# Optimization experiments

Measured on AMD Instinct MI355X. Metric: run time of the kernel, lower is better.

## Reference

```python
import jax, jax.numpy as jnp
import numpy as np
from jax import lax


def setup_inputs() -> dict:
    key = jax.random.key(0)
    ks = jax.random.split(key, 8)
    b, l, d_model = 2, 1024, 768
    expand, d_state, d_conv = 2, 16, 4
    d_inner = d_model * expand            # 1536
    dt_rank = -(-d_model // 16)           # ceil(768/16) = 48
    x = jax.random.normal(ks[0], (b, l, d_model), jnp.float32)
    W_in = jax.random.normal(ks[1], (d_model, 2 * d_inner), jnp.float32) * 0.02
    conv_w = jax.random.normal(ks[2], (d_inner, 1, d_conv), jnp.float32) * 0.1
    conv_b = jnp.zeros((d_inner,), jnp.float32)
    W_x = jax.random.normal(ks[3], (d_inner, dt_rank + 2 * d_state), jnp.float32) * 0.02
    W_dt = jax.random.normal(ks[4], (dt_rank, d_inner), jnp.float32) * 0.02
    b_dt = jax.random.normal(ks[5], (d_inner,), jnp.float32) * 0.02
    # A_log = log(1..d_state) broadcast over d_inner, as in the module init
    A_log = jnp.broadcast_to(jnp.log(jnp.arange(1, d_state + 1, dtype=jnp.float32)), (d_inner, d_state)).copy()
    D = jnp.ones((d_inner,), jnp.float32)
    W_out = jax.random.normal(ks[6], (d_inner, d_model), jnp.float32) * 0.02
    return {"x": x, "W_in": W_in, "conv_w": conv_w, "conv_b": conv_b, "W_x": W_x,
            "W_dt": W_dt, "b_dt": b_dt, "A_log": A_log, "D": D, "W_out": W_out}


def _silu(v):
    return v * jax.nn.sigmoid(v)


def reference(x, W_in, conv_w, conv_b, W_x, W_dt, b_dt, A_log, D, W_out):
    b, l, d_model = x.shape
    d_inner, _, d_conv = conv_w.shape
    dt_rank = W_dt.shape[0]
    n = A_log.shape[1]

    # in_proj and split into x / res paths
    x_and_res = x @ W_in                              # (b, l, 2*d_inner)
    xi, res = jnp.split(x_and_res, 2, axis=-1)

    # depthwise causal conv1d (torch pads d_conv-1 both sides then slices [:l])
    xc = jnp.transpose(xi, (0, 2, 1))                 # (b, d_inner, l)
    xc = lax.conv_general_dilated(
        xc, conv_w, window_strides=(1,), padding=[(d_conv - 1, 0)],
        dimension_numbers=("NCH", "OIH", "NCH"), feature_group_count=d_inner)
    xc = xc + conv_b[None, :, None]
    u = _silu(jnp.transpose(xc, (0, 2, 1)))           # (b, l, d_inner)

    # SSM parameters (input-dependent)
    A = -jnp.exp(A_log.astype(jnp.float32))           # (d_inner, n)
    x_dbl = u @ W_x                                   # (b, l, dt_rank + 2n)
    delta = x_dbl[..., :dt_rank]
    B = x_dbl[..., dt_rank:dt_rank + n]               # (b, l, n)
    C = x_dbl[..., dt_rank + n:]                      # (b, l, n)
    delta = jax.nn.softplus(delta @ W_dt + b_dt)      # (b, l, d_inner)

    # discretize
    deltaA = jnp.exp(delta[..., None] * A)            # (b, l, d_inner, n)
    deltaB_u = delta[..., None] * B[:, :, None, :] * u[..., None]  # (b, l, d_inner, n)

    # parallel associative scan over l: h_t = deltaA_t * h_{t-1} + deltaB_u_t
    def combine(c1, c2):
        a1, b1 = c1
        a2, b2 = c2
        return (a1 * a2, a2 * b1 + b2)

    _, hs = lax.associative_scan(combine, (deltaA, deltaB_u), axis=1)  # (b, l, d_inner, n)

    y = jnp.einsum("bldn,bln->bld", hs, C) + u * D    # (b, l, d_inner)
    y = y * _silu(res)
    out = y @ W_out                                   # (b, l, d_model)
    return out
```

## Files before the change

### kernel.cpp

```cpp
#include <hip/hip_runtime.h>
#include <math.h>

#define DI 1536
#define DM 768
#define NSTATE 16
#define DTRANK 48
#define LSEQ 1024
#define NBATCH 2
#define MROWS (NBATCH*LSEQ)
#define NXR 3072
#define NCHUNK 64
#define CLEN 16
#define SCB 128
#define DMP 16

typedef __attribute__((ext_vector_type(4))) float f32x4;
typedef __attribute__((ext_vector_type(8))) short s16x8;
typedef __attribute__((ext_vector_type(4))) unsigned int u32x4;

__device__ __forceinline__ unsigned short f2bf(float f) {
  unsigned int x = __builtin_bit_cast(unsigned int, f);
  return (unsigned short)((x + 0x7fffu + ((x >> 16) & 1u)) >> 16);
}

__device__ __forceinline__ void gload_lds16(const void* g, void* l) {
  __builtin_amdgcn_global_load_lds(
      (const __attribute__((address_space(1))) void*)g,
      (__attribute__((address_space(3))) void*)l, 16, 0, 0);
}

__global__ __launch_bounds__(256) void convert_bf16_kernel(
    const float* __restrict__ in, unsigned short* __restrict__ out, long n)
{
  long i = ((long)blockIdx.x * 256 + threadIdx.x) * 8;
  if (i >= n) return;
  f32x4 v0 = *(const f32x4*)&in[i];
  f32x4 v1 = *(const f32x4*)&in[i + 4];
  unsigned short o[8];
  #pragma unroll
  for (int j = 0; j < 4; ++j) { o[j] = f2bf(v0[j]); o[4 + j] = f2bf(v1[j]); }
  *(u32x4*)&out[i] = *(u32x4*)o;
}

__global__ __launch_bounds__(256) void transpose_bf16_kernel(
    const float* __restrict__ in, unsigned short* __restrict__ out, int R, int C)
{
  __shared__ float t[32][33];
  int ctile = blockIdx.x * 32, rtile = blockIdx.y * 32;
  int tx = threadIdx.x & 31, ty = threadIdx.x >> 5;
  #pragma unroll
  for (int i = 0; i < 4; ++i) {
    int r = ty + i * 8;
    t[r][tx] = in[(long)(rtile + r) * C + ctile + tx];
  }
  __syncthreads();
  #pragma unroll
  for (int i = 0; i < 4; ++i) {
    int cc = ty + i * 8;
    out[(long)(ctile + cc) * R + rtile + tx] = f2bf(t[tx][cc]);
  }
}

__global__ __launch_bounds__(256) void transpose_bf16_guard(
    const float* __restrict__ in, unsigned short* __restrict__ out, int R, int C)
{
  __shared__ float t[32][33];
  int ctile = blockIdx.x * 32, rtile = blockIdx.y * 32;
  int tx = threadIdx.x & 31, ty = threadIdx.x >> 5;
  #pragma unroll
  for (int i = 0; i < 4; ++i) {
    int r = ty + i * 8;
    if (rtile + r < R && ctile + tx < C)
      t[r][tx] = in[(long)(rtile + r) * C + ctile + tx];
  }
  __syncthreads();
  #pragma unroll
  for (int i = 0; i < 4; ++i) {
    int cc = ty + i * 8;
    if (ctile + cc < C && rtile + tx < R)
      out[(long)(ctile + cc) * R + rtile + tx] = f2bf(t[tx][cc]);
  }
}

template<int FM, int FN>
__global__ __launch_bounds__(256) void gemm_bf16(
    const unsigned short* __restrict__ A,
    const unsigned short* __restrict__ BT,
    float* __restrict__ C, int M, int N, int K)
{
  constexpr int BM = 32 * FM, BN = 32 * FN;
  constexpr int TM = BM / 16, TN = BN / 16;
  __shared__ unsigned short Ap[BM * 32];
  __shared__ unsigned short Bp[BN * 32];
  const int tid = threadIdx.x;
  const int lane = tid & 63, wave = tid >> 6;
  const int wr = wave >> 1, wc = wave & 1;
  const int lg = lane >> 4, lr = lane & 15;
  const int m0 = blockIdx.y * BM, n0 = blockIdx.x * BN;
  f32x4 acc[FM][FN] = {};
  for (int k0 = 0; k0 < K; k0 += 32) {
    #pragma unroll
    for (int p = 0; p < TM / 4; ++p) {
      int tile = wave + p * 4;
      gload_lds16(&A[(long)(m0 + tile * 16 + lr) * K + k0 + lg * 8],
                  &Ap[tile * 512]);
    }
    #pragma unroll
    for (int p = 0; p < TN / 4; ++p) {
      int tile = wave + p * 4;
      gload_lds16(&BT[(long)(n0 + tile * 16 + lr) * K + k0 + lg * 8],
                  &Bp[tile * 512]);
    }
    __syncthreads();
    s16x8 af[FM], bfr[FN];
    #pragma unroll
    for (int m = 0; m < FM; ++m)
      af[m] = *(s16x8*)&Ap[(((wr * FM + m) * 4 + lg) * 16 + lr) * 8];
    #pragma unroll
    for (int n = 0; n < FN; ++n)
      bfr[n] = *(s16x8*)&Bp[(((wc * FN + n) * 4 + lg) * 16 + lr) * 8];
    #pragma unroll
    for (int m = 0; m < FM; ++m)
      #pragma unroll
      for (int n = 0; n < FN; ++n)
        acc[m][n] = __builtin_amdgcn_mfma_f32_16x16x32_bf16(af[m], bfr[n], acc[m][n], 0, 0, 0);
    __syncthreads();
  }
  #pragma unroll
  for (int m = 0; m < FM; ++m)
    #pragma unroll
    for (int n = 0; n < FN; ++n)
      #pragma unroll
      for (int r = 0; r < 4; ++r) {
        int row = m0 + wr * 16 * FM + m * 16 + lg * 4 + r;
        int col = n0 + wc * 16 * FN + n * 16 + lr;
        C[(long)row * N + col] = acc[m][n][r];
      }
}

__global__ __launch_bounds__(256) void conv_silu_kernel(
    const float* __restrict__ xr,
    const float* __restrict__ conv_w,
    const float* __restrict__ conv_b,
    float* __restrict__ u,
    unsigned short* __restrict__ u_bf)
{
  int idx = blockIdx.x * 256 + threadIdx.x;
  if (idx >= MROWS * DI) return;
  int c = idx % DI;
  int bm = idx / DI;
  int t = bm % LSEQ;
  int b = bm / LSEQ;
  float w0 = conv_w[c * 4 + 0], w1 = conv_w[c * 4 + 1];
  float w2 = conv_w[c * 4 + 2], w3 = conv_w[c * 4 + 3];
  const float* xc = xr + (long)b * LSEQ * NXR + c;
  float acc = conv_b[c];
  if (t >= 3) acc = fmaf(xc[(long)(t - 3) * NXR], w0, acc);
  if (t >= 2) acc = fmaf(xc[(long)(t - 2) * NXR], w1, acc);
  if (t >= 1) acc = fmaf(xc[(long)(t - 1) * NXR], w2, acc);
  acc = fmaf(xc[(long)t * NXR], w3, acc);
  float s = acc / (1.f + __expf(-acc));
  u[idx] = s;
  u_bf[idx] = f2bf(s);
}

__global__ __launch_bounds__(256) void xdbl_mfma(
    const unsigned short* __restrict__ u_bf,
    const unsigned short* __restrict__ WxT,
    float* __restrict__ xdbl)
{
  const int tid = threadIdx.x;
  const int lane = tid & 63, wave = tid >> 6;
  const int lg = lane >> 4, lr = lane & 15;
  const int m0 = blockIdx.x * 16;
  f32x4 acc[5] = {};
  const int kbase = wave * (DI / 4);
  #pragma unroll
  for (int kk = 0; kk < DI / 4; kk += 32) {
    int k0 = kbase + kk;
    s16x8 af = *(const s16x8*)&u_bf[(long)(m0 + lr) * DI + k0 + lg * 8];
    #pragma unroll
    for (int n = 0; n < 5; ++n) {
      s16x8 bfr = *(const s16x8*)&WxT[(long)(n * 16 + lr) * DI + k0 + lg * 8];
      acc[n] = __builtin_amdgcn_mfma_f32_16x16x32_bf16(af, bfr, acc[n], 0, 0, 0);
    }
  }
  __shared__ float red[4][16][80];
  #pragma unroll
  for (int n = 0; n < 5; ++n)
    #pragma unroll
    for (int r = 0; r < 4; ++r)
      red[wave][lg * 4 + r][n * 16 + lr] = acc[n][r];
  __syncthreads();
  for (int i = tid; i < 16 * 80; i += 256) {
    int row = i / 80, col = i % 80;
    float s = red[0][row][col] + red[1][row][col] + red[2][row][col] + red[3][row][col];
    xdbl[(long)(m0 + row) * 80 + col] = s;
  }
}

__global__ __launch_bounds__(256) void delta_kernel(
    const float* __restrict__ xdbl,
    const float* __restrict__ W_dt,
    const float* __restrict__ b_dt,
    float* __restrict__ delta)
{
  __shared__ float sx[DMP][DTRANK];
  const int tid = threadIdx.x;
  const int c = blockIdx.x * 256 + tid;
  const int m0 = blockIdx.y * DMP;
  for (int i = tid; i < DMP * DTRANK; i += 256) {
    int mm = i / DTRANK, r = i % DTRANK;
    sx[mm][r] = xdbl[(long)(m0 + mm) * 80 + r];
  }
  __syncthreads();
  float bias = b_dt[c];
  float acc[DMP];
  #pragma unroll
  for (int mm = 0; mm < DMP; ++mm) acc[mm] = bias;
  for (int r = 0; r < DTRANK; ++r) {
    float wv = W_dt[(long)r * DI + c];
    #pragma unroll
    for (int mm = 0; mm < DMP; ++mm)
      acc[mm] = fmaf(sx[mm][r], wv, acc[mm]);
  }
  #pragma unroll
  for (int mm = 0; mm < DMP; ++mm) {
    float v = acc[mm];
    float sp = (v > 20.f) ? v : log1pf(__expf(v));
    delta[(long)(m0 + mm) * DI + c] = sp;
  }
}

__global__ __launch_bounds__(SCB) void scan_ph1(
    const float* __restrict__ delta,
    const float* __restrict__ xdbl,
    const float* __restrict__ u,
    const float* __restrict__ A_log,
    float* __restrict__ Aprod,
    float* __restrict__ Hend)
{
  const int b = blockIdx.z, chunk = blockIdx.y;
  const int tid = threadIdx.x;
  const int d = blockIdx.x * SCB + tid;
  const long mbase = (long)b * LSEQ + chunk * CLEN;
  __shared__ float sB[CLEN][NSTATE];
  for (int i = tid; i < CLEN * NSTATE; i += SCB) {
    int t = i >> 4, j = i & 15;
    sB[t][j] = xdbl[(mbase + t) * 80 + DTRANK + j];
  }
  __syncthreads();
  float a[NSTATE];
  #pragma unroll
  for (int n = 0; n < NSTATE; ++n)
    a[n] = -__expf(A_log[(long)d * NSTATE + n]);
  float h[NSTATE] = {};
  float Ap[NSTATE];
  #pragma unroll
  for (int n = 0; n < NSTATE; ++n) Ap[n] = 1.f;
  #pragma unroll 4
  for (int t = 0; t < CLEN; ++t) {
    long m = mbase + t;
    float dt = delta[m * DI + d];
    float uu = u[m * DI + d];
    float dtu = dt * uu;
    #pragma unroll
    for (int n = 0; n < NSTATE; ++n) {
      float dA = __expf(dt * a[n]);
      Ap[n] *= dA;
      h[n] = fmaf(dA, h[n], dtu * sB[t][n]);
    }
  }
  long o = (((long)b * NCHUNK + chunk) * DI + d) * NSTATE;
  #pragma unroll
  for (int q = 0; q < 4; ++q) {
    f32x4 va = { Ap[q*4+0], Ap[q*4+1], Ap[q*4+2], Ap[q*4+3] };
    f32x4 vh = { h[q*4+0], h[q*4+1], h[q*4+2], h[q*4+3] };
    *(f32x4*)&Aprod[o + q*4] = va;
    *(f32x4*)&Hend[o + q*4] = vh;
  }
}

__global__ __launch_bounds__(256) void scan_ph2(
    const float* __restrict__ Aprod,
    const float* __restrict__ Hend,
    float* __restrict__ Hstart)
{
  int idx = blockIdx.x * 256 + threadIdx.x;
  int b = idx / (DI * NSTATE);
  int r = idx % (DI * NSTATE);
  long o = (long)b * NCHUNK * DI * NSTATE + r;
  const long stride = (long)DI * NSTATE;
  float h = 0.f;
  for (int c = 0; c < NCHUNK; ++c) {
    float Ap = Aprod[o + c * stride];
    float He = Hend[o + c * stride];
    Hstart[o + c * stride] = h;
    h = fmaf(Ap, h, He);
  }
}

__global__ __launch_bounds__(SCB) void scan_ph3(
    const float* __restrict__ delta,
    const float* __restrict__ xdbl,
    const float* __restrict__ u,
    const float* __restrict__ xr,
    const float* __restrict__ A_log,
    const float* __restrict__ Dp,
    const float* __restrict__ Hstart,
    unsigned short* __restrict__ yg)
{
  const int b = blockIdx.z, chunk = blockIdx.y;
  const int tid = threadIdx.x;
  const int d = blockIdx.x * SCB + tid;
  const long mbase = (long)b * LSEQ + chunk * CLEN;
  __shared__ float sB[CLEN][NSTATE], sC[CLEN][NSTATE];
  for (int i = tid; i < CLEN * NSTATE; i += SCB) {
    int t = i >> 4, j = i & 15;
    long mo = (mbase + t) * 80 + DTRANK + j;
    sB[t][j] = xdbl[mo];
    sC[t][j] = xdbl[mo + NSTATE];
  }
  __syncthreads();
  float a[NSTATE];
  #pragma unroll
  for (int n = 0; n < NSTATE; ++n)
    a[n] = -__expf(A_log[(long)d * NSTATE + n]);
  const float Dv = Dp[d];
  long o = (((long)b * NCHUNK + chunk) * DI + d) * NSTATE;
  float h[NSTATE];
  #pragma unroll
  for (int q = 0; q < 4; ++q) {
    f32x4 vh = *(const f32x4*)&Hstart[o + q*4];
    h[q*4+0] = vh[0]; h[q*4+1] = vh[1]; h[q*4+2] = vh[2]; h[q*4+3] = vh[3];
  }
  #pragma unroll 4
  for (int t = 0; t < CLEN; ++t) {
    long m = mbase + t;
    float dt = delta[m * DI + d];
    float uu = u[m * DI + d];
    float rr = xr[m * NXR + DI + d];
    float dtu = dt * uu;
    float p0 = 0.f, p1 = 0.f, p2 = 0.f, p3 = 0.f;
    #pragma unroll
    for (int q = 0; q < 4; ++q) {
      float dA0 = __expf(dt * a[q*4+0]);
      float dA1 = __expf(dt * a[q*4+1]);
      float dA2 = __expf(dt * a[q*4+2]);
      float dA3 = __expf(dt * a[q*4+3]);
      h[q*4+0] = fmaf(dA0, h[q*4+0], dtu * sB[t][q*4+0]);
      h[q*4+1] = fmaf(dA1, h[q*4+1], dtu * sB[t][q*4+1]);
      h[q*4+2] = fmaf(dA2, h[q*4+2], dtu * sB[t][q*4+2]);
      h[q*4+3] = fmaf(dA3, h[q*4+3], dtu * sB[t][q*4+3]);
    }
    #pragma unroll
    for (int n = 0; n < NSTATE; n += 4) {
      p0 = fmaf(h[n+0], sC[t][n+0], p0);
      p1 = fmaf(h[n+1], sC[t][n+1], p1);
      p2 = fmaf(h[n+2], sC[t][n+2], p2);
      p3 = fmaf(h[n+3], sC[t][n+3], p3);
    }
    float yv = (p0 + p1) + (p2 + p3) + uu * Dv;
    float gate = rr / (1.f + __expf(-rr));
    yg[m * DI + d] = f2bf(yv * gate);
  }
}

extern "C" void kernel_launch(void* const* d_in, const int* in_sizes, int n_in,
                              void* d_out, int out_size, void* d_ws, size_t ws_size,
                              hipStream_t stream)
{
  const float* x      = (const float*)d_in[0];
  const float* W_in   = (const float*)d_in[1];
  const float* conv_w = (const float*)d_in[2];
  const float* conv_b = (const float*)d_in[3];
  const float* W_x    = (const float*)d_in[4];
  const float* W_dt   = (const float*)d_in[5];
  const float* b_dt   = (const float*)d_in[6];
  const float* A_log  = (const float*)d_in[7];
  const float* Dp     = (const float*)d_in[8];
  const float* W_out  = (const float*)d_in[9];
  float* out = (float*)d_out;

  char* p = (char*)d_ws;
  float* xr     = (float*)(p + 0);
  float* u      = (float*)(p + 25165824);
  float* xdbl   = (float*)(p + 37748736);
  float* delta  = (float*)(p + 38404096);
  float* Aprod  = (float*)(p + 50987008);
  float* Hend   = (float*)(p + 63569920);
  unsigned short* yg    = (unsigned short*)(p + 76152832);
  unsigned short* WoutT = (unsigned short*)(p + 82444288);
  float* Hstart = (float*)(p + 84803584);
  unsigned short* x_bf = (unsigned short*)delta;
  unsigned short* WinT = (unsigned short*)Aprod;
  unsigned short* u_bf = (unsigned short*)Hend;
  unsigned short* WxT  = (unsigned short*)Hstart;

  convert_bf16_kernel<<<(MROWS * DM) / (256 * 8), 256, 0, stream>>>(x, x_bf, (long)MROWS * DM);
  transpose_bf16_kernel<<<dim3(NXR / 32, DM / 32), 256, 0, stream>>>(W_in, WinT, DM, NXR);
  transpose_bf16_kernel<<<dim3(DM / 32, DI / 32), 256, 0, stream>>>(W_out, WoutT, DI, DM);
  transpose_bf16_guard<<<dim3(3, DI / 32), 256, 0, stream>>>(W_x, WxT, DI, 80);
  gemm_bf16<4, 4><<<dim3(NXR / 128, MROWS / 128), 256, 0, stream>>>(
      x_bf, WinT, xr, MROWS, NXR, DM);
  conv_silu_kernel<<<(MROWS * DI + 255) / 256, 256, 0, stream>>>(xr, conv_w, conv_b, u, u_bf);
  xdbl_mfma<<<MROWS / 16, 256, 0, stream>>>(u_bf, WxT, xdbl);
  delta_kernel<<<dim3(DI / 256, MROWS / DMP), 256, 0, stream>>>(xdbl, W_dt, b_dt, delta);
  scan_ph1<<<dim3(DI / SCB, NCHUNK, NBATCH), SCB, 0, stream>>>(delta, xdbl, u, A_log, Aprod, Hend);
  scan_ph2<<<(NBATCH * DI * NSTATE) / 256, 256, 0, stream>>>(Aprod, Hend, Hstart);
  scan_ph3<<<dim3(DI / SCB, NCHUNK, NBATCH), SCB, 0, stream>>>(
      delta, xdbl, u, xr, A_log, Dp, Hstart, yg);
  gemm_bf16<2, 2><<<dim3(DM / 64, MROWS / 64), 256, 0, stream>>>(
      yg, WoutT, out, MROWS, DM, DI);
}
```

Baseline: 176.2 us.

## Merge prep kernels into one launch and double scan chunk count

The bf16 conversion of x and the three weight transposes are merged into a single prep kernel dispatched by block index, cutting three launches. The chunked scan now uses 128 chunks of 8 steps instead of 64 of 16, which doubles the number of parallel blocks in phases 1 and 3 and fully unrolls their inner time loop. The workspace is laid out again with separate, larger Aprod/Hend/Hstart buffers instead of aliased ones. The cost is that the sequential phase 2 combine and the chunk-state traffic both double.

```diff
diff --git a/kernel.cpp b/kernel.cpp
--- a/kernel.cpp
+++ b/kernel.cpp
@@ -9,8 +9,8 @@
 #define NBATCH 2
 #define MROWS (NBATCH*LSEQ)
 #define NXR 3072
-#define NCHUNK 64
-#define CLEN 16
+#define NCHUNK 128
+#define CLEN 8
 #define SCB 128
 #define DMP 16
 
@@ -29,55 +29,42 @@
       (__attribute__((address_space(3))) void*)l, 16, 0, 0);
 }
 
-__global__ __launch_bounds__(256) void convert_bf16_kernel(
-    const float* __restrict__ in, unsigned short* __restrict__ out, long n)
-{
-  long i = ((long)blockIdx.x * 256 + threadIdx.x) * 8;
-  if (i >= n) return;
-  f32x4 v0 = *(const f32x4*)&in[i];
-  f32x4 v1 = *(const f32x4*)&in[i + 4];
-  unsigned short o[8];
-  #pragma unroll
-  for (int j = 0; j < 4; ++j) { o[j] = f2bf(v0[j]); o[4 + j] = f2bf(v1[j]); }
-  *(u32x4*)&out[i] = *(u32x4*)o;
-}
-
-__global__ __launch_bounds__(256) void transpose_bf16_kernel(
-    const float* __restrict__ in, unsigned short* __restrict__ out, int R, int C)
+__global__ __launch_bounds__(256) void prep_kernel(
+    const float* __restrict__ x, const float* __restrict__ W_in,
+    const float* __restrict__ W_out, const float* __restrict__ W_x,
+    unsigned short* __restrict__ x_bf, unsigned short* __restrict__ WinT,
+    unsigned short* __restrict__ WoutT, unsigned short* __restrict__ WxT)
 {
   __shared__ float t[32][33];
-  int ctile = blockIdx.x * 32, rtile = blockIdx.y * 32;
-  int tx = threadIdx.x & 31, ty = threadIdx.x >> 5;
+  const int bid = blockIdx.x;
+  const int tid = threadIdx.x;
+  if (bid < 768) {
+    long i = ((long)bid * 256 + tid) * 8;
+    f32x4 v0 = *(const f32x4*)&x[i];
+    f32x4 v1 = *(const f32x4*)&x[i + 4];
+    unsigned short o[8];
+    #pragma unroll
+    for (int j = 0; j < 4; ++j) { o[j] = f2bf(v0[j]); o[4 + j] = f2bf(v1[j]); }
+    *(u32x4*)&x_bf[i] = *(u32x4*)o;
+    return;
+  }
+  const float* in; unsigned short* out; int R, C, bx, by; bool guard = false;
+  if (bid < 3072)      { int q = bid - 768;  in = W_in;  out = WinT;  R = DM; C = NXR; bx = q % 96; by = q / 96; }
+  else if (bid < 4224) { int q = bid - 3072; in = W_out; out = WoutT; R = DI; C = DM;  bx = q % 24; by = q / 24; }
+  else                 { int q = bid - 4224; in = W_x;   out = WxT;   R = DI; C = 80;  bx = q % 3;  by = q / 3; guard = true; }
+  int ctile = bx * 32, rtile = by * 32;
+  int tx = tid & 31, ty = tid >> 5;
   #pragma unroll
   for (int i = 0; i < 4; ++i) {
     int r = ty + i * 8;
-    t[r][tx] = in[(long)(rtile + r) * C + ctile + tx];
+    if (!guard || (rtile + r < R && ctile + tx < C))
+      t[r][tx] = in[(long)(rtile + r) * C + ctile + tx];
   }
   __syncthreads();
   #pragma unroll
   for (int i = 0; i < 4; ++i) {
     int cc = ty + i * 8;
-    out[(long)(ctile + cc) * R + rtile + tx] = f2bf(t[tx][cc]);
-  }
-}
-
-__global__ __launch_bounds__(256) void transpose_bf16_guard(
-    const float* __restrict__ in, unsigned short* __restrict__ out, int R, int C)
-{
-  __shared__ float t[32][33];
-  int ctile = blockIdx.x * 32, rtile = blockIdx.y * 32;
-  int tx = threadIdx.x & 31, ty = threadIdx.x >> 5;
-  #pragma unroll
-  for (int i = 0; i < 4; ++i) {
-    int r = ty + i * 8;
-    if (rtile + r < R && ctile + tx < C)
-      t[r][tx] = in[(long)(rtile + r) * C + ctile + tx];
-  }
-  __syncthreads();
-  #pragma unroll
-  for (int i = 0; i < 4; ++i) {
-    int cc = ty + i * 8;
-    if (ctile + cc < C && rtile + tx < R)
+    if (!guard || (ctile + cc < C && rtile + tx < R))
       out[(long)(ctile + cc) * R + rtile + tx] = f2bf(t[tx][cc]);
   }
 }
@@ -102,14 +89,12 @@
     #pragma unroll
     for (int p = 0; p < TM / 4; ++p) {
       int tile = wave + p * 4;
-      gload_lds16(&A[(long)(m0 + tile * 16 + lr) * K + k0 + lg * 8],
-                  &Ap[tile * 512]);
+      gload_lds16(&A[(long)(m0 + tile * 16 + lr) * K + k0 + lg * 8], &Ap[tile * 512]);
     }
     #pragma unroll
     for (int p = 0; p < TN / 4; ++p) {
       int tile = wave + p * 4;
-      gload_lds16(&BT[(long)(n0 + tile * 16 + lr) * K + k0 + lg * 8],
-                  &Bp[tile * 512]);
+      gload_lds16(&BT[(long)(n0 + tile * 16 + lr) * K + k0 + lg * 8], &Bp[tile * 512]);
     }
     __syncthreads();
     s16x8 af[FM], bfr[FN];
@@ -258,7 +243,7 @@
   float Ap[NSTATE];
   #pragma unroll
   for (int n = 0; n < NSTATE; ++n) Ap[n] = 1.f;
-  #pragma unroll 4
+  #pragma unroll
   for (int t = 0; t < CLEN; ++t) {
     long m = mbase + t;
     float dt = delta[m * DI + d];
@@ -334,7 +319,7 @@
     f32x4 vh = *(const f32x4*)&Hstart[o + q*4];
     h[q*4+0] = vh[0]; h[q*4+1] = vh[1]; h[q*4+2] = vh[2]; h[q*4+3] = vh[3];
   }
-  #pragma unroll 4
+  #pragma unroll
   for (int t = 0; t < CLEN; ++t) {
     long m = mbase + t;
     float dt = delta[m * DI + d];
@@ -385,28 +370,26 @@
   char* p = (char*)d_ws;
   float* xr     = (float*)(p + 0);
   float* u      = (float*)(p + 25165824);
-  float* xdbl   = (float*)(p + 37748736);
-  float* delta  = (float*)(p + 38404096);
-  float* Aprod  = (float*)(p + 50987008);
-  float* Hend   = (float*)(p + 63569920);
-  unsigned short* yg    = (unsigned short*)(p + 76152832);
-  unsigned short* WoutT = (unsigned short*)(p + 82444288);
-  float* Hstart = (float*)(p + 84803584);
-  unsigned short* x_bf = (unsigned short*)delta;
-  unsigned short* WinT = (unsigned short*)Aprod;
-  unsigned short* u_bf = (unsigned short*)Hend;
-  unsigned short* WxT  = (unsigned short*)Hstart;
-
-  convert_bf16_kernel<<<(MROWS * DM) / (256 * 8), 256, 0, stream>>>(x, x_bf, (long)MROWS * DM);
-  transpose_bf16_kernel<<<dim3(NXR / 32, DM / 32), 256, 0, stream>>>(W_in, WinT, DM, NXR);
-  transpose_bf16_kernel<<<dim3(DM / 32, DI / 32), 256, 0, stream>>>(W_out, WoutT, DI, DM);
-  transpose_bf16_guard<<<dim3(3, DI / 32), 256, 0, stream>>>(W_x, WxT, DI, 80);
+  unsigned short* u_bf = (unsigned short*)(p + 37748736);
+  float* xdbl   = (float*)(p + 44040192);
+  float* delta  = (float*)(p + 44695552);
+  float* Aprod  = (float*)(p + 57278464);
+  float* Hend   = (float*)(p + 82444288);
+  float* Hstart = (float*)(p + 107610112);
+  unsigned short* yg    = (unsigned short*)(p + 132775936);
+  unsigned short* x_bf  = (unsigned short*)(p + 139067392);
+  unsigned short* WinT  = (unsigned short*)(p + 142213120);
+  unsigned short* WoutT = (unsigned short*)(p + 146931712);
+  unsigned short* WxT   = (unsigned short*)(p + 149291008);
+
+  prep_kernel<<<4368, 256, 0, stream>>>(x, W_in, W_out, W_x, x_bf, WinT, WoutT, WxT);
   gemm_bf16<4, 4><<<dim3(NXR / 128, MROWS / 128), 256, 0, stream>>>(
       x_bf, WinT, xr, MROWS, NXR, DM);
   conv_silu_kernel<<<(MROWS * DI + 255) / 256, 256, 0, stream>>>(xr, conv_w, conv_b, u, u_bf);
   xdbl_mfma<<<MROWS / 16, 256, 0, stream>>>(u_bf, WxT, xdbl);
   delta_kernel<<<dim3(DI / 256, MROWS / DMP), 256, 0, stream>>>(xdbl, W_dt, b_dt, delta);
-  scan_ph1<<<dim3(DI / SCB, NCHUNK, NBATCH), SCB, 0, stream>>>(delta, xdbl, u, A_log, Aprod, Hend);
+  scan_ph1<<<dim3(DI / SCB, NCHUNK, NBATCH), SCB, 0, stream>>>(
+      delta, xdbl, u, A_log, Aprod, Hend);
   scan_ph2<<<(NBATCH * DI * NSTATE) / 256, 256, 0, stream>>>(Aprod, Hend, Hstart);
   scan_ph3<<<dim3(DI / SCB, NCHUNK, NBATCH), SCB, 0, stream>>>(
       delta, xdbl, u, xr, A_log, Dp, Hstart, yg);
```

Result: faster. 166.9 us (-5.3%).
